# Optimization experiments

Measured on AMD Instinct MI355X. Metric: run time of the kernel, lower is better.

The kernel has to match this reference:

```python
import jax, jax.numpy as jnp
import numpy as np

B, T, D, H, L, V = 2, 1024, 1024, 4, 4, 32000  # H redefined below
H = 16            # n_heads
HD = D // H       # head_size = 64
NL = 4            # n_layer
EPS = 1e-5


def _layernorm(x, scale, bias):
    mu = jnp.mean(x, axis=-1, keepdims=True)
    var = jnp.mean(jnp.square(x - mu), axis=-1, keepdims=True)
    return (x - mu) * jax.lax.rsqrt(var + EPS) * scale + bias


def setup_inputs() -> dict:
    key = jax.random.key(0)
    ks = iter(jax.random.split(key, 40))
    s = lambda shape: jax.random.normal(next(ks), shape, jnp.float32) * 0.02
    inp = {
        'idx': jax.random.randint(next(ks), (B, T), 0, V),
        'tok_emb': s((V, D)),
        'pos_emb': s((T, D)),
        # per-layer stacked params (leading axis = layer)
        'Wq': s((NL, D, D)), 'Wk': s((NL, D, D)), 'Wv': s((NL, D, D)),
        'Wo': s((NL, D, D)), 'bo': jnp.zeros((NL, D), jnp.float32),
        'ln1_s': jnp.ones((NL, D), jnp.float32), 'ln1_b': jnp.zeros((NL, D), jnp.float32),
        'ln2_s': jnp.ones((NL, D), jnp.float32), 'ln2_b': jnp.zeros((NL, D), jnp.float32),
        'W1': s((NL, D, 4 * D)), 'b1': jnp.zeros((NL, 4 * D), jnp.float32),
        'W2': s((NL, 4 * D, D)), 'b2': jnp.zeros((NL, D), jnp.float32),
        'lnf_s': jnp.ones((D,), jnp.float32), 'lnf_b': jnp.zeros((D,), jnp.float32),
        'Wlm': s((D, V)), 'blm': jnp.zeros((V,), jnp.float32),
    }
    return inp


def reference(idx, tok_emb, pos_emb, Wq, Wk, Wv, Wo, bo,
              ln1_s, ln1_b, ln2_s, ln2_b, W1, b1, W2, b2,
              lnf_s, lnf_b, Wlm, blm):
    b, t = idx.shape
    x = tok_emb[idx] + pos_emb[None, :t]            # [B,T,D]
    causal = jnp.tril(jnp.ones((t, t), bool))        # [T,T]
    scale = 1.0 / np.sqrt(HD).astype(np.float32)
    for l in range(NL):
        h = _layernorm(x, ln1_s[l], ln1_b[l])
        q = (h @ Wq[l]).reshape(b, t, H, HD)
        k = (h @ Wk[l]).reshape(b, t, H, HD)
        v = (h @ Wv[l]).reshape(b, t, H, HD)
        scores = jnp.einsum('bthd,bshd->bhts', q, k) * scale
        scores = jnp.where(causal[None, None], scores, -jnp.inf)
        attn = jax.nn.softmax(scores, axis=-1)       # [B,H,T,T]
        o = jnp.einsum('bhts,bshd->bthd', attn, v).reshape(b, t, D)
        x = x + o @ Wo[l] + bo[l]
        h2 = _layernorm(x, ln2_s[l], ln2_b[l])
        x = x + jax.nn.relu(h2 @ W1[l] + b1[l]) @ W2[l] + b2[l]
    x = _layernorm(x, lnf_s, lnf_b)
    logits = x @ Wlm + blm                           # [B,T,V]
    return logits
```

## Files before the change

### kernel.cpp

```cpp
#include <hip/hip_runtime.h>

typedef unsigned short u16;
typedef unsigned int u32;
typedef __bf16 bf16x8 __attribute__((ext_vector_type(8)));
typedef float f32x4 __attribute__((ext_vector_type(4)));
typedef u16 u16x8 __attribute__((ext_vector_type(8)));
typedef u16 u16x4 __attribute__((ext_vector_type(4)));

static __device__ __forceinline__ u16 f2bf(float f) {
  u32 u = __builtin_bit_cast(u32, f);
  u32 r = (u + 0x7FFFu + ((u >> 16) & 1u)) >> 16;
  return (u16)r;
}

#define GLOAD_LDS16(gp, lp)                                                   \
  __builtin_amdgcn_global_load_lds(                                           \
      (const __attribute__((address_space(1))) void*)(gp),                    \
      (__attribute__((address_space(3))) void*)(lp), 16, 0, 0)

__global__ void k_embed(const int* __restrict__ idx, const float* __restrict__ tok,
                        const float* __restrict__ pos, float* __restrict__ x) {
  int row = blockIdx.x;
  int t = row & 1023;
  int id = idx[row];
  int c = threadIdx.x * 4;
  float4 a = *(const float4*)(tok + (size_t)id * 1024 + c);
  float4 p = *(const float4*)(pos + (size_t)t * 1024 + c);
  float4 r{a.x + p.x, a.y + p.y, a.z + p.z, a.w + p.w};
  *(float4*)(x + (size_t)row * 1024 + c) = r;
}

__global__ void k_ln(const float* __restrict__ x, const float* __restrict__ sc,
                     const float* __restrict__ bi, u16* __restrict__ out) {
  int row = blockIdx.x;
  int t = threadIdx.x;
  const float* xr = x + (size_t)row * 1024;
  float4 v = *(const float4*)(xr + t * 4);
  float s = v.x + v.y + v.z + v.w;
  float ss = v.x * v.x + v.y * v.y + v.z * v.z + v.w * v.w;
  for (int d = 1; d < 64; d <<= 1) { s += __shfl_xor(s, d); ss += __shfl_xor(ss, d); }
  __shared__ float red[8];
  int wave = t >> 6, lane = t & 63;
  if (lane == 0) { red[wave] = s; red[wave + 4] = ss; }
  __syncthreads();
  s = red[0] + red[1] + red[2] + red[3];
  ss = red[4] + red[5] + red[6] + red[7];
  float mu = s * (1.0f / 1024.0f);
  float var = ss * (1.0f / 1024.0f) - mu * mu;
  float inv = rsqrtf(var + 1e-5f);
  float4 g = *(const float4*)(sc + t * 4);
  float4 b = *(const float4*)(bi + t * 4);
  u16x4 o;
  o[0] = f2bf((v.x - mu) * inv * g.x + b.x);
  o[1] = f2bf((v.y - mu) * inv * g.y + b.y);
  o[2] = f2bf((v.z - mu) * inv * g.z + b.z);
  o[3] = f2bf((v.w - mu) * inv * g.w + b.w);
  *(u16x4*)(out + (size_t)row * 1024 + t * 4) = o;
}

__launch_bounds__(1024)
__global__ void k_transpose(const float* __restrict__ src, u16* __restrict__ dst,
                            int R, int C) {
  __shared__ float tile[32][33];
  int tx = threadIdx.x, ty = threadIdx.y;
  int c = blockIdx.x * 32 + tx;
  int r = blockIdx.y * 32 + ty;
  tile[ty][tx] = src[(size_t)r * C + c];
  __syncthreads();
  int dr = blockIdx.x * 32 + ty;
  int dc = blockIdx.y * 32 + tx;
  dst[(size_t)dr * R + dc] = f2bf(tile[tx][ty]);
}

__launch_bounds__(1024)
__global__ void k_transpose_layer(const float* __restrict__ Wq, const float* __restrict__ Wk,
                                  const float* __restrict__ Wv, const float* __restrict__ Wo,
                                  const float* __restrict__ W1, const float* __restrict__ W2,
                                  u16* __restrict__ qkvT, u16* __restrict__ WoT,
                                  u16* __restrict__ W1T, u16* __restrict__ W2T) {
  int bid = blockIdx.x;
  const float* src; u16* dst; int R, C, bx, by;
  if (bid < 4096) {
    int which = bid >> 10, tile_i = bid & 1023;
    bx = tile_i & 31; by = tile_i >> 5; R = 1024; C = 1024;
    src = which == 0 ? Wq : which == 1 ? Wk : which == 2 ? Wv : Wo;
    dst = which == 3 ? WoT : qkvT + (size_t)which * 1048576;
  } else if (bid < 8192) {
    int tile_i = bid - 4096; bx = tile_i & 127; by = tile_i >> 7; R = 1024; C = 4096;
    src = W1; dst = W1T;
  } else {
    int tile_i = bid - 8192; bx = tile_i & 31; by = tile_i >> 5; R = 4096; C = 1024;
    src = W2; dst = W2T;
  }
  __shared__ float tile[32][33];
  int tx = threadIdx.x, ty = threadIdx.y;
  int c = bx * 32 + tx, r = by * 32 + ty;
  tile[ty][tx] = src[(size_t)r * C + c];
  __syncthreads();
  int dr = bx * 32 + ty, dc = by * 32 + tx;
  dst[(size_t)dr * R + dc] = f2bf(tile[tx][ty]);
}

enum { EPI_QKV = 0, EPI_RES = 1, EPI_RELU = 2 };

template <int EPI>
__launch_bounds__(256, 4)
__global__ void k_gemm(const u16* __restrict__ A, const u16* __restrict__ Bt,
                       const float* __restrict__ bias, float* __restrict__ fout,
                       u16* __restrict__ bout, int M, int N, int K) {
  __shared__ alignas(16) u16 sm[2][2][128][32];
  const int t = threadIdx.x;
  const int wave = t >> 6, lane = t & 63;
  const int wm = wave >> 1, wn = wave & 1;
  const int g = lane >> 4, c = lane & 15;
  const int m0 = blockIdx.x * 128, n0 = blockIdx.y * 128;

  const int srow = wave * 32 + (lane >> 2);
  const int sseg = (lane & 3) * 8;
  const u16* gA = A + (size_t)(m0 + srow) * K + sseg;
  const u16* gB = Bt + (size_t)(n0 + srow) * K + sseg;

  f32x4 acc[4][4] = {};
  const int nK = K >> 5;
  int cur = 0;

#pragma unroll
  for (int p = 0; p < 2; ++p) {
    GLOAD_LDS16(gA + (size_t)p * 16 * K, &sm[0][0][wave * 32 + p * 16][0]);
    GLOAD_LDS16(gB + (size_t)p * 16 * K, &sm[0][1][wave * 32 + p * 16][0]);
  }
  __syncthreads();

  for (int kt = 0; kt < nK; ++kt) {
    if (kt + 1 < nK) {
      const int k0 = (kt + 1) << 5;
#pragma unroll
      for (int p = 0; p < 2; ++p) {
        GLOAD_LDS16(gA + k0 + (size_t)p * 16 * K, &sm[cur ^ 1][0][wave * 32 + p * 16][0]);
        GLOAD_LDS16(gB + k0 + (size_t)p * 16 * K, &sm[cur ^ 1][1][wave * 32 + p * 16][0]);
      }
    }
    bf16x8 af[4], bfr[4];
#pragma unroll
    for (int i = 0; i < 4; ++i) {
      af[i]  = *(const bf16x8*)&sm[cur][0][wm * 64 + i * 16 + c][g * 8];
      bfr[i] = *(const bf16x8*)&sm[cur][1][wn * 64 + i * 16 + c][g * 8];
    }
#pragma unroll
    for (int i = 0; i < 4; ++i)
#pragma unroll
      for (int j = 0; j < 4; ++j)
        acc[i][j] = __builtin_amdgcn_mfma_f32_16x16x32_bf16(af[i], bfr[j], acc[i][j], 0, 0, 0);
    __syncthreads();
    cur ^= 1;
  }

#pragma unroll
  for (int i = 0; i < 4; ++i)
#pragma unroll
    for (int j = 0; j < 4; ++j)
#pragma unroll
      for (int r = 0; r < 4; ++r) {
        int m = m0 + wm * 64 + i * 16 + g * 4 + r;
        int n = n0 + wn * 64 + j * 16 + c;
        float v = acc[i][j][r];
        if (EPI == EPI_RES) {
          fout[(size_t)m * N + n] += v + bias[n];
        } else if (EPI == EPI_RELU) {
          float u = v + bias[n];
          bout[(size_t)m * N + n] = f2bf(u > 0.f ? u : 0.f);
        }
      }
}

template <int EPI>
__launch_bounds__(256, 4)
__global__ void k_gemm64(const u16* __restrict__ A, const u16* __restrict__ Bt,
                         const float* __restrict__ bias, float* __restrict__ fout,
                         u16* __restrict__ bout, int M, int N, int K) {
  __shared__ alignas(16) u16 smem[12288];
#define AL(s, r, k) smem[(s)*2048 + (r)*32 + (k)]
#define BL(s, r, k) smem[4096 + (s)*4096 + (r)*32 + (k)]
  const int t = threadIdx.x;
  const int wave = t >> 6, lane = t & 63;
  const int wm = wave >> 1, wn = wave & 1;
  const int g = lane >> 4, c = lane & 15;
  const int m0 = blockIdx.x * 64, n0 = blockIdx.y * 128;

  const int rwA = t >> 2, sgA = (t & 3) * 8;
  const u16* gA = A + (size_t)(m0 + rwA) * K + sgA;
  const u16* gB = Bt + (size_t)(n0 + rwA) * K + sgA;

  f32x4 acc[2][4] = {};
  const int nK = K >> 5;
  int cur = 0;

  GLOAD_LDS16(gA, &AL(0, rwA, 0));
#pragma unroll
  for (int p = 0; p < 2; ++p)
    GLOAD_LDS16(gB + (size_t)p * 64 * K, &BL(0, p * 64 + rwA, 0));
  __syncthreads();

  for (int kt = 0; kt < nK; ++kt) {
    if (kt + 1 < nK) {
      const int k0 = (kt + 1) << 5;
      GLOAD_LDS16(gA + k0, &AL(cur ^ 1, rwA, 0));
#pragma unroll
      for (int p = 0; p < 2; ++p)
        GLOAD_LDS16(gB + k0 + (size_t)p * 64 * K, &BL(cur ^ 1, p * 64 + rwA, 0));
    }
    bf16x8 af[2], bfr[4];
#pragma unroll
    for (int i = 0; i < 2; ++i)
      af[i] = *(const bf16x8*)&AL(cur, wm * 32 + i * 16 + c, g * 8);
#pragma unroll
    for (int j = 0; j < 4; ++j)
      bfr[j] = *(const bf16x8*)&BL(cur, wn * 64 + j * 16 + c, g * 8);
#pragma unroll
    for (int i = 0; i < 2; ++i)
#pragma unroll
      for (int j = 0; j < 4; ++j)
        acc[i][j] = __builtin_amdgcn_mfma_f32_16x16x32_bf16(af[i], bfr[j], acc[i][j], 0, 0, 0);
    __syncthreads();
    cur ^= 1;
  }

  if (EPI == EPI_QKV) {
    u16 (*Ct)[136] = (u16(*)[136])smem;
#pragma unroll
    for (int i = 0; i < 2; ++i)
#pragma unroll
      for (int j = 0; j < 4; ++j)
#pragma unroll
        for (int r = 0; r < 4; ++r)
          Ct[wm * 32 + i * 16 + g * 4 + r][wn * 64 + j * 16 + c] = f2bf(acc[i][j][r]);
    __syncthreads();
    const int b = m0 >> 10, t0 = m0 & 1023;
    const int hh0 = (n0 >> 6) & 15, which = n0 >> 10;
    u16* obase = bout + (size_t)which * 2097152;
#pragma unroll
    for (int itr = 0; itr < 4; ++itr) {
      int idx2 = itr * 256 + t;
      int s = idx2 >> 9;
      int tt = (idx2 >> 3) & 63;
      int seg = idx2 & 7;
      u16x8 vv = *(const u16x8*)&Ct[tt][s * 64 + seg * 8];
      *(u16x8*)(obase + ((size_t)(b * 16 + hh0 + s) * 1024 + (t0 + tt)) * 64 + seg * 8) = vv;
    }
    return;
  }

#pragma unroll
  for (int i = 0; i < 2; ++i)
#pragma unroll
    for (int j = 0; j < 4; ++j)
#pragma unroll
      for (int r = 0; r < 4; ++r) {
        int m = m0 + wm * 32 + i * 16 + g * 4 + r;
        int n = n0 + wn * 64 + j * 16 + c;
        if (EPI == EPI_RES) fout[(size_t)m * N + n] += acc[i][j][r] + bias[n];
      }
#undef AL
#undef BL
}


#define BAR                                                                    \
  {                                                                            \
    asm volatile("" ::: "memory");                                             \
    __builtin_amdgcn_s_barrier();                                              \
    asm volatile("" ::: "memory");                                             \
  }
#define VM4 asm volatile("s_waitcnt vmcnt(4)" ::: "memory")
#define VM0 asm volatile("s_waitcnt vmcnt(0)" ::: "memory")

#define STGA(sl, hf, kt)                                                       \
  {                                                                            \
    _Pragma("unroll") for (int p = 0; p < 2; ++p) {                            \
      int idx = p * 512 + t, rw = idx >> 3, sg = idx & 7;                      \
      GLOAD_LDS16(A + (size_t)(m0 + (hf)*128 + rw) * K + (kt)*64 +             \
                      ((sg ^ (rw & 7)) << 3),                                  \
                  &Alds[sl][(hf)*128 + rw][sg << 3]);                          \
    }                                                                          \
  }
#define STGB(sl, hf, kt)                                                       \
  {                                                                            \
    _Pragma("unroll") for (int p = 0; p < 2; ++p) {                            \
      int idx = p * 512 + t, rw = idx >> 3, sg = idx & 7;                      \
      GLOAD_LDS16(Bt + (size_t)(n0 + (hf)*128 + rw) * K + (kt)*64 +            \
                      ((sg ^ (rw & 7)) << 3),                                  \
                  &Blds[sl][(hf)*128 + rw][sg << 3]);                          \
    }                                                                          \
  }

#define LMLOAD_A(sl, mh)                                                       \
  _Pragma("unroll") for (int i = 0; i < 4; ++i) {                              \
    int ra = (mh)*128 + wm * 64 + i * 16 + c;                                  \
    _Pragma("unroll") for (int ks = 0; ks < 2; ++ks)                           \
      af[i][ks] = *(const bf16x8*)&Alds[sl][ra][(((ks << 2) | g) ^ (ra & 7)) << 3]; \
  }
#define LMLOAD_B(sl, nh, bfv)                                                  \
  _Pragma("unroll") for (int j = 0; j < 2; ++j) {                              \
    int rb = (nh)*128 + wn * 32 + j * 16 + c;                                  \
    _Pragma("unroll") for (int ks = 0; ks < 2; ++ks)                           \
      bfv[j][ks] = *(const bf16x8*)&Blds[sl][rb][(((ks << 2) | g) ^ (rb & 7)) << 3]; \
  }
#define LMMMA(mh, nh, bfv)                                                     \
  __builtin_amdgcn_s_setprio(1);                                               \
  _Pragma("unroll") for (int i = 0; i < 4; ++i)                                \
    _Pragma("unroll") for (int j = 0; j < 2; ++j)                              \
      _Pragma("unroll") for (int ks = 0; ks < 2; ++ks)                         \
        acc[mh][nh][i][j] = __builtin_amdgcn_mfma_f32_16x16x32_bf16(           \
            af[i][ks], bfv[j][ks], acc[mh][nh][i][j], 0, 0, 0);                \
  __builtin_amdgcn_s_setprio(0);

__launch_bounds__(512, 2)
__global__ void k_gemm_lm(const u16* __restrict__ A, const u16* __restrict__ Bt,
                          const float* __restrict__ bias, float* __restrict__ fout,
                          int M, int N, int K) {
  __shared__ alignas(16) u16 Alds[2][256][64];
  __shared__ alignas(16) u16 Blds[2][256][64];
  const int t = threadIdx.x;
  const int wid = t >> 6, lane = t & 63;
  const int wm = wid >> 2, wn = wid & 3;
  const int g = lane >> 4, c = lane & 15;

  int bid = blockIdx.x;
  int swz = (bid & 7) * 125 + (bid >> 3);
  const int m0 = (swz & 7) * 256, n0 = (swz >> 3) * 256;

  f32x4 acc[2][2][4][2] = {};
  bf16x8 af[4][2], bf0[2][2], bf1[2][2];

  const int nK = K >> 6;
  const int nIter = nK >> 1;

  STGA(0, 0, 0); STGB(0, 0, 0);
  STGA(0, 1, 0); STGB(0, 1, 0);
  STGA(1, 0, 1); STGB(1, 0, 1);
  VM4;
  BAR;

  for (int it = 0; it < nIter; ++it) {
    const int t1 = 2 * it + 1, t2 = 2 * it + 2, t3 = 2 * it + 3;
    const bool more = (it + 1 < nIter);
    LMLOAD_A(0, 0); LMLOAD_B(0, 0, bf0);
    STGA(1, 1, t1); STGB(1, 1, t1);
    BAR; LMMMA(0, 0, bf0); BAR;
    LMLOAD_B(0, 1, bf1);
    BAR; LMMMA(0, 1, bf1); BAR;
    LMLOAD_A(0, 1);
    if (more) { STGA(0, 0, t2); }
    BAR; LMMMA(1, 1, bf1); BAR;
    if (more) { STGB(0, 0, t2); BAR; LMMMA(1, 0, bf0); VM4; BAR; }
    else      { BAR; LMMMA(1, 0, bf0); VM0; BAR; }
    LMLOAD_A(1, 0); LMLOAD_B(1, 0, bf0);
    if (more) { STGA(0, 1, t2); STGB(0, 1, t2); }
    BAR; LMMMA(0, 0, bf0); BAR;
    LMLOAD_B(1, 1, bf1);
    BAR; LMMMA(0, 1, bf1); BAR;
    LMLOAD_A(1, 1);
    if (more) { STGA(1, 0, t3); STGB(1, 0, t3); }
    BAR; LMMMA(1, 1, bf1); BAR;
    if (more) { BAR; LMMMA(1, 0, bf0); VM4; BAR; }
    else      { BAR; LMMMA(1, 0, bf0); VM0; BAR; }
  }

  float (*stile)[260] = (float(*)[260])&Alds[0][0][0];
#pragma unroll
  for (int RG = 0; RG < 8; ++RG) {
    const int mh = RG >> 2, wsel = (RG >> 1) & 1, ih = RG & 1;
    if (wm == wsel) {
#pragma unroll
      for (int i2 = 0; i2 < 2; ++i2)
#pragma unroll
        for (int nh = 0; nh < 2; ++nh)
#pragma unroll
          for (int j = 0; j < 2; ++j)
#pragma unroll
            for (int r = 0; r < 4; ++r) {
              float v = acc[mh][nh][ih * 2 + i2][j][r];
              stile[i2 * 16 + g * 4 + r][nh * 128 + wn * 32 + j * 16 + c] = v;
            }
    }
    __syncthreads();
    {
      int row = t >> 4, seg = t & 15;
      int m = m0 + RG * 32 + row;
      float* dst = fout + (size_t)m * N + n0 + seg * 16;
      const float* bsrc = bias + n0 + seg * 16;
#pragma unroll
      for (int q = 0; q < 4; ++q) {
        float4 v = *(const float4*)&stile[row][seg * 16 + q * 4];
        float4 bb = *(const float4*)&bsrc[q * 4];
        float4 o{v.x + bb.x, v.y + bb.y, v.z + bb.z, v.w + bb.w};
        *(float4*)(dst + q * 4) = o;
      }
    }
    __syncthreads();
  }
}

__launch_bounds__(64)
__global__ void k_attn(const u16* __restrict__ Q, const u16* __restrict__ Kb,
                       const u16* __restrict__ V, u16* __restrict__ O) {
  const int qb = blockIdx.x;
  const int bh = blockIdx.y;
  const int lane = threadIdx.x;
  const int g = lane >> 4, c = lane & 15;
  const int q0 = qb << 5;
  const u16* Qh = Q + (size_t)bh * 65536;
  const u16* Kh = Kb + (size_t)bh * 65536;
  const u16* Vh = V + (size_t)bh * 65536;

  __shared__ u16 Vt[64][40];
  __shared__ u16 Pl[32][40];

  bf16x8 aq[2][2];
#pragma unroll
  for (int qt = 0; qt < 2; ++qt) {
    aq[qt][0] = *(const bf16x8*)(Qh + (q0 + qt * 16 + c) * 64 + g * 8);
    aq[qt][1] = *(const bf16x8*)(Qh + (q0 + qt * 16 + c) * 64 + 32 + g * 8);
  }

  f32x4 Oacc[2][4] = {};
  float Mr[2][4], Lr[2][4] = {};
#pragma unroll
  for (int qt = 0; qt < 2; ++qt)
#pragma unroll
    for (int r = 0; r < 4; ++r) Mr[qt][r] = -1e30f;

  const int nIt = qb + 1;
  for (int it = 0; it < nIt; ++it) {
    const int k0 = it << 5;
    bf16x8 b0 = *(const bf16x8*)(Kh + (k0 + c) * 64 + g * 8);
    bf16x8 b1 = *(const bf16x8*)(Kh + (k0 + c) * 64 + 32 + g * 8);
    bf16x8 b2 = *(const bf16x8*)(Kh + (k0 + 16 + c) * 64 + g * 8);
    bf16x8 b3 = *(const bf16x8*)(Kh + (k0 + 16 + c) * 64 + 32 + g * 8);
    f32x4 S[2][2];
#pragma unroll
    for (int qt = 0; qt < 2; ++qt) {
      f32x4 z = {};
      S[qt][0] = __builtin_amdgcn_mfma_f32_16x16x32_bf16(
          aq[qt][1], b1, __builtin_amdgcn_mfma_f32_16x16x32_bf16(aq[qt][0], b0, z, 0, 0, 0), 0, 0, 0);
      S[qt][1] = __builtin_amdgcn_mfma_f32_16x16x32_bf16(
          aq[qt][1], b3, __builtin_amdgcn_mfma_f32_16x16x32_bf16(aq[qt][0], b2, z, 0, 0, 0), 0, 0, 0);
    }
#pragma unroll
    for (int p = 0; p < 4; ++p) {
      int key = (p << 3) + (lane >> 3);
      int d0 = (lane & 7) << 3;
      u16x8 vv = *(const u16x8*)(Vh + (size_t)(k0 + key) * 64 + d0);
#pragma unroll
      for (int j = 0; j < 8; ++j) Vt[d0 + j][key] = vv[j];
    }
    const float scale = 0.125f;
#pragma unroll
    for (int qt = 0; qt < 2; ++qt)
#pragma unroll
      for (int r = 0; r < 4; ++r) {
        int q = q0 + qt * 16 + (g << 2) + r;
        float s0 = (k0 + c <= q) ? S[qt][0][r] * scale : -1e30f;
        float s1 = (k0 + 16 + c <= q) ? S[qt][1][r] * scale : -1e30f;
        float m = fmaxf(s0, s1);
        m = fmaxf(m, __shfl_xor(m, 1));
        m = fmaxf(m, __shfl_xor(m, 2));
        m = fmaxf(m, __shfl_xor(m, 4));
        m = fmaxf(m, __shfl_xor(m, 8));
        float mnew = fmaxf(Mr[qt][r], m);
        float p0 = __expf(s0 - mnew);
        float p1 = __expf(s1 - mnew);
        float rs = p0 + p1;
        rs += __shfl_xor(rs, 1);
        rs += __shfl_xor(rs, 2);
        rs += __shfl_xor(rs, 4);
        rs += __shfl_xor(rs, 8);
        float alpha = __expf(Mr[qt][r] - mnew);
        Lr[qt][r] = Lr[qt][r] * alpha + rs;
        Mr[qt][r] = mnew;
#pragma unroll
        for (int nb = 0; nb < 4; ++nb) Oacc[qt][nb][r] *= alpha;
        Pl[qt * 16 + (g << 2) + r][c] = f2bf(p0);
        Pl[qt * 16 + (g << 2) + r][16 + c] = f2bf(p1);
      }
#pragma unroll
    for (int nb = 0; nb < 4; ++nb) {
      bf16x8 bv = *(const bf16x8*)&Vt[nb * 16 + c][g * 8];
#pragma unroll
      for (int qt = 0; qt < 2; ++qt) {
        bf16x8 ap = *(const bf16x8*)&Pl[qt * 16 + c][g * 8];
        Oacc[qt][nb] = __builtin_amdgcn_mfma_f32_16x16x32_bf16(ap, bv, Oacc[qt][nb], 0, 0, 0);
      }
    }
  }
  const int b = bh >> 4, hh = bh & 15;
#pragma unroll
  for (int qt = 0; qt < 2; ++qt)
#pragma unroll
    for (int r = 0; r < 4; ++r) {
      int tt = q0 + qt * 16 + (g << 2) + r;
      float invl = 1.0f / Lr[qt][r];
#pragma unroll
      for (int nb = 0; nb < 4; ++nb) {
        int d = nb * 16 + c;
        O[((size_t)(b * 1024 + tt)) * 1024 + hh * 64 + d] = f2bf(Oacc[qt][nb][r] * invl);
      }
    }
}

extern "C" void kernel_launch(void* const* d_in, const int* in_sizes, int n_in,
                              void* d_out, int out_size, void* d_ws, size_t ws_size,
                              hipStream_t stream) {
  const int*   idx  = (const int*)d_in[0];
  const float* tok  = (const float*)d_in[1];
  const float* pos  = (const float*)d_in[2];
  const float* Wq   = (const float*)d_in[3];
  const float* Wk   = (const float*)d_in[4];
  const float* Wv   = (const float*)d_in[5];
  const float* Wo   = (const float*)d_in[6];
  const float* bo   = (const float*)d_in[7];
  const float* ln1s = (const float*)d_in[8];
  const float* ln1b = (const float*)d_in[9];
  const float* ln2s = (const float*)d_in[10];
  const float* ln2b = (const float*)d_in[11];
  const float* W1   = (const float*)d_in[12];
  const float* b1   = (const float*)d_in[13];
  const float* W2   = (const float*)d_in[14];
  const float* b2   = (const float*)d_in[15];
  const float* lnfs = (const float*)d_in[16];
  const float* lnfb = (const float*)d_in[17];
  const float* Wlm  = (const float*)d_in[18];
  const float* blm  = (const float*)d_in[19];
  float* out = (float*)d_out;

  char* w = (char*)d_ws;
  auto alloc = [&](size_t bytes) {
    char* p = w;
    w += (bytes + 255) & ~(size_t)255;
    return p;
  };
  float* x  = (float*)alloc(2048ull * 1024 * 4);
  u16* h    = (u16*)alloc(2048ull * 1024 * 2);
  u16* qkv  = (u16*)alloc(3ull * 2097152 * 2);
  u16* o    = (u16*)alloc(2048ull * 1024 * 2);
  u16* a1   = (u16*)alloc(2048ull * 4096 * 2);
  u16* arena = (u16*)alloc(32000ull * 1024 * 2);

  dim3 b32(32, 32, 1);

  k_embed<<<2048, 256, 0, stream>>>(idx, tok, pos, x);

  for (int l = 0; l < 4; ++l) {
    u16* qkvT = arena;
    u16* WoT  = arena + 3ull * 1048576;
    u16* W1T  = arena + 4ull * 1048576;
    u16* W2T  = arena + 8ull * 1048576;
    k_transpose_layer<<<12288, b32, 0, stream>>>(
        Wq + (size_t)l * 1048576, Wk + (size_t)l * 1048576,
        Wv + (size_t)l * 1048576, Wo + (size_t)l * 1048576,
        W1 + (size_t)l * 4194304, W2 + (size_t)l * 4194304,
        qkvT, WoT, W1T, W2T);

    k_ln<<<2048, 256, 0, stream>>>(x, ln1s + l * 1024, ln1b + l * 1024, h);
    k_gemm64<EPI_QKV><<<dim3(32, 24), 256, 0, stream>>>(h, qkvT, nullptr, nullptr, qkv,
                                                        2048, 3072, 1024);
    k_attn<<<dim3(32, 32), 64, 0, stream>>>(qkv, qkv + 2097152, qkv + 2 * 2097152, o);
    k_gemm64<EPI_RES><<<dim3(32, 8), 256, 0, stream>>>(o, WoT, bo + l * 1024, x, nullptr,
                                                       2048, 1024, 1024);
    k_ln<<<2048, 256, 0, stream>>>(x, ln2s + l * 1024, ln2b + l * 1024, h);
    k_gemm<EPI_RELU><<<dim3(16, 32), 256, 0, stream>>>(h, W1T, b1 + l * 4096, nullptr, a1,
                                                       2048, 4096, 1024);
    k_gemm64<EPI_RES><<<dim3(32, 8), 256, 0, stream>>>(a1, W2T, b2 + l * 1024, x, nullptr,
                                                       2048, 1024, 4096);
  }

  k_ln<<<2048, 256, 0, stream>>>(x, lnfs, lnfb, h);
  k_transpose<<<dim3(1000, 32), b32, 0, stream>>>(Wlm, arena, 1024, 32000);
  k_gemm_lm<<<1000, 512, 0, stream>>>(h, arena, blm, out, 2048, 32000, 1024);
}
```

Measured before the change: 1.270 ms.

## Retile GEMMs, replace LM-head kernel, add lazy softmax rescale in attention

The hand-pipelined 256x256 LM-head GEMM with 512 threads is replaced by a simpler 128x128 double-buffered kernel that writes logits through an LDS-staged epilogue. The residual GEMMs (Wo and W2) move to a new 64x64-tile kernel so twice as many blocks cover the small N=1024 output. The W1 ReLU GEMM moves to the 64x128 kernel with an LDS-staged, vectorised bf16 store. Attention skips the running-max update and the output rescale when no row's max has grown by more than 8, trading some exponent headroom for fewer exp and multiply operations. Several independent changes carry different risks; the simpler LM-head kernel is the largest and may be slower than the tuned version it replaces.

```diff
diff --git a/kernel.cpp b/kernel.cpp
--- a/kernel.cpp
+++ b/kernel.cpp
@@ -101,83 +101,13 @@
   dst[(size_t)dr * R + dc] = f2bf(tile[tx][ty]);
 }
 
-enum { EPI_QKV = 0, EPI_RES = 1, EPI_RELU = 2 };
-
-template <int EPI>
-__launch_bounds__(256, 4)
-__global__ void k_gemm(const u16* __restrict__ A, const u16* __restrict__ Bt,
-                       const float* __restrict__ bias, float* __restrict__ fout,
-                       u16* __restrict__ bout, int M, int N, int K) {
-  __shared__ alignas(16) u16 sm[2][2][128][32];
-  const int t = threadIdx.x;
-  const int wave = t >> 6, lane = t & 63;
-  const int wm = wave >> 1, wn = wave & 1;
-  const int g = lane >> 4, c = lane & 15;
-  const int m0 = blockIdx.x * 128, n0 = blockIdx.y * 128;
-
-  const int srow = wave * 32 + (lane >> 2);
-  const int sseg = (lane & 3) * 8;
-  const u16* gA = A + (size_t)(m0 + srow) * K + sseg;
-  const u16* gB = Bt + (size_t)(n0 + srow) * K + sseg;
-
-  f32x4 acc[4][4] = {};
-  const int nK = K >> 5;
-  int cur = 0;
-
-#pragma unroll
-  for (int p = 0; p < 2; ++p) {
-    GLOAD_LDS16(gA + (size_t)p * 16 * K, &sm[0][0][wave * 32 + p * 16][0]);
-    GLOAD_LDS16(gB + (size_t)p * 16 * K, &sm[0][1][wave * 32 + p * 16][0]);
-  }
-  __syncthreads();
-
-  for (int kt = 0; kt < nK; ++kt) {
-    if (kt + 1 < nK) {
-      const int k0 = (kt + 1) << 5;
-#pragma unroll
-      for (int p = 0; p < 2; ++p) {
-        GLOAD_LDS16(gA + k0 + (size_t)p * 16 * K, &sm[cur ^ 1][0][wave * 32 + p * 16][0]);
-        GLOAD_LDS16(gB + k0 + (size_t)p * 16 * K, &sm[cur ^ 1][1][wave * 32 + p * 16][0]);
-      }
-    }
-    bf16x8 af[4], bfr[4];
-#pragma unroll
-    for (int i = 0; i < 4; ++i) {
-      af[i]  = *(const bf16x8*)&sm[cur][0][wm * 64 + i * 16 + c][g * 8];
-      bfr[i] = *(const bf16x8*)&sm[cur][1][wn * 64 + i * 16 + c][g * 8];
-    }
-#pragma unroll
-    for (int i = 0; i < 4; ++i)
-#pragma unroll
-      for (int j = 0; j < 4; ++j)
-        acc[i][j] = __builtin_amdgcn_mfma_f32_16x16x32_bf16(af[i], bfr[j], acc[i][j], 0, 0, 0);
-    __syncthreads();
-    cur ^= 1;
-  }
-
-#pragma unroll
-  for (int i = 0; i < 4; ++i)
-#pragma unroll
-    for (int j = 0; j < 4; ++j)
-#pragma unroll
-      for (int r = 0; r < 4; ++r) {
-        int m = m0 + wm * 64 + i * 16 + g * 4 + r;
-        int n = n0 + wn * 64 + j * 16 + c;
-        float v = acc[i][j][r];
-        if (EPI == EPI_RES) {
-          fout[(size_t)m * N + n] += v + bias[n];
-        } else if (EPI == EPI_RELU) {
-          float u = v + bias[n];
-          bout[(size_t)m * N + n] = f2bf(u > 0.f ? u : 0.f);
-        }
-      }
-}
+enum { EPI_QKV = 0, EPI_RELU = 2 };
 
 template <int EPI>
 __launch_bounds__(256, 4)
 __global__ void k_gemm64(const u16* __restrict__ A, const u16* __restrict__ Bt,
-                         const float* __restrict__ bias, float* __restrict__ fout,
-                         u16* __restrict__ bout, int M, int N, int K) {
+                         const float* __restrict__ bias, u16* __restrict__ bout,
+                         int M, int N, int K) {
   __shared__ alignas(16) u16 smem[12288];
 #define AL(s, r, k) smem[(s)*2048 + (r)*32 + (k)]
 #define BL(s, r, k) smem[4096 + (s)*4096 + (r)*32 + (k)]
@@ -247,152 +177,156 @@
       u16x8 vv = *(const u16x8*)&Ct[tt][s * 64 + seg * 8];
       *(u16x8*)(obase + ((size_t)(b * 16 + hh0 + s) * 1024 + (t0 + tt)) * 64 + seg * 8) = vv;
     }
-    return;
+  } else {
+    u16 (*Ct)[136] = (u16(*)[136])smem;
+#pragma unroll
+    for (int i = 0; i < 2; ++i)
+#pragma unroll
+      for (int j = 0; j < 4; ++j)
+#pragma unroll
+        for (int r = 0; r < 4; ++r) {
+          float u = acc[i][j][r] + bias[n0 + wn * 64 + j * 16 + c];
+          Ct[wm * 32 + i * 16 + g * 4 + r][wn * 64 + j * 16 + c] = f2bf(u > 0.f ? u : 0.f);
+        }
+    __syncthreads();
+#pragma unroll
+    for (int itr = 0; itr < 4; ++itr) {
+      int idx2 = itr * 256 + t;
+      int tt = idx2 >> 4, seg = idx2 & 15;
+      *(u16x8*)(bout + (size_t)(m0 + tt) * N + n0 + seg * 8) =
+          *(const u16x8*)&Ct[tt][seg * 8];
+    }
+  }
+#undef AL
+#undef BL
+}
+
+__launch_bounds__(256, 8)
+__global__ void k_gemm_res(const u16* __restrict__ A, const u16* __restrict__ Bt,
+                           const float* __restrict__ bias, float* __restrict__ fout,
+                           int M, int N, int K) {
+  __shared__ alignas(16) u16 smem[8192];
+  const int t = threadIdx.x;
+  const int wave = t >> 6, lane = t & 63;
+  const int wm = wave >> 1, wn = wave & 1;
+  const int g = lane >> 4, c = lane & 15;
+  const int m0 = blockIdx.x * 64, n0 = blockIdx.y * 64;
+
+  const int rw = t >> 2, sg = (t & 3) * 8;
+  const u16* gA = A + (size_t)(m0 + rw) * K + sg;
+  const u16* gB = Bt + (size_t)(n0 + rw) * K + sg;
+
+  f32x4 acc[2][2] = {};
+  const int nK = K >> 5;
+  int cur = 0;
+
+  GLOAD_LDS16(gA, &smem[rw * 32]);
+  GLOAD_LDS16(gB, &smem[4096 + rw * 32]);
+  __syncthreads();
+
+  for (int kt = 0; kt < nK; ++kt) {
+    if (kt + 1 < nK) {
+      const int k0 = (kt + 1) << 5;
+      GLOAD_LDS16(gA + k0, &smem[(cur ^ 1) * 2048 + rw * 32]);
+      GLOAD_LDS16(gB + k0, &smem[4096 + (cur ^ 1) * 2048 + rw * 32]);
+    }
+    bf16x8 af[2], bfr[2];
+#pragma unroll
+    for (int i = 0; i < 2; ++i)
+      af[i] = *(const bf16x8*)&smem[cur * 2048 + (wm * 32 + i * 16 + c) * 32 + g * 8];
+#pragma unroll
+    for (int j = 0; j < 2; ++j)
+      bfr[j] = *(const bf16x8*)&smem[4096 + cur * 2048 + (wn * 32 + j * 16 + c) * 32 + g * 8];
+#pragma unroll
+    for (int i = 0; i < 2; ++i)
+#pragma unroll
+      for (int j = 0; j < 2; ++j)
+        acc[i][j] = __builtin_amdgcn_mfma_f32_16x16x32_bf16(af[i], bfr[j], acc[i][j], 0, 0, 0);
+    __syncthreads();
+    cur ^= 1;
   }
 
 #pragma unroll
   for (int i = 0; i < 2; ++i)
 #pragma unroll
-    for (int j = 0; j < 4; ++j)
+    for (int j = 0; j < 2; ++j)
 #pragma unroll
       for (int r = 0; r < 4; ++r) {
         int m = m0 + wm * 32 + i * 16 + g * 4 + r;
-        int n = n0 + wn * 64 + j * 16 + c;
-        if (EPI == EPI_RES) fout[(size_t)m * N + n] += acc[i][j][r] + bias[n];
-      }
-#undef AL
-#undef BL
-}
-
-
-#define BAR                                                                    \
-  {                                                                            \
-    asm volatile("" ::: "memory");                                             \
-    __builtin_amdgcn_s_barrier();                                              \
-    asm volatile("" ::: "memory");                                             \
-  }
-#define VM4 asm volatile("s_waitcnt vmcnt(4)" ::: "memory")
-#define VM0 asm volatile("s_waitcnt vmcnt(0)" ::: "memory")
-
-#define STGA(sl, hf, kt)                                                       \
-  {                                                                            \
-    _Pragma("unroll") for (int p = 0; p < 2; ++p) {                            \
-      int idx = p * 512 + t, rw = idx >> 3, sg = idx & 7;                      \
-      GLOAD_LDS16(A + (size_t)(m0 + (hf)*128 + rw) * K + (kt)*64 +             \
-                      ((sg ^ (rw & 7)) << 3),                                  \
-                  &Alds[sl][(hf)*128 + rw][sg << 3]);                          \
-    }                                                                          \
-  }
-#define STGB(sl, hf, kt)                                                       \
-  {                                                                            \
-    _Pragma("unroll") for (int p = 0; p < 2; ++p) {                            \
-      int idx = p * 512 + t, rw = idx >> 3, sg = idx & 7;                      \
-      GLOAD_LDS16(Bt + (size_t)(n0 + (hf)*128 + rw) * K + (kt)*64 +            \
-                      ((sg ^ (rw & 7)) << 3),                                  \
-                  &Blds[sl][(hf)*128 + rw][sg << 3]);                          \
-    }                                                                          \
-  }
-
-#define LMLOAD_A(sl, mh)                                                       \
-  _Pragma("unroll") for (int i = 0; i < 4; ++i) {                              \
-    int ra = (mh)*128 + wm * 64 + i * 16 + c;                                  \
-    _Pragma("unroll") for (int ks = 0; ks < 2; ++ks)                           \
-      af[i][ks] = *(const bf16x8*)&Alds[sl][ra][(((ks << 2) | g) ^ (ra & 7)) << 3]; \
-  }
-#define LMLOAD_B(sl, nh, bfv)                                                  \
-  _Pragma("unroll") for (int j = 0; j < 2; ++j) {                              \
-    int rb = (nh)*128 + wn * 32 + j * 16 + c;                                  \
-    _Pragma("unroll") for (int ks = 0; ks < 2; ++ks)                           \
-      bfv[j][ks] = *(const bf16x8*)&Blds[sl][rb][(((ks << 2) | g) ^ (rb & 7)) << 3]; \
-  }
-#define LMMMA(mh, nh, bfv)                                                     \
-  __builtin_amdgcn_s_setprio(1);                                               \
-  _Pragma("unroll") for (int i = 0; i < 4; ++i)                                \
-    _Pragma("unroll") for (int j = 0; j < 2; ++j)                              \
-      _Pragma("unroll") for (int ks = 0; ks < 2; ++ks)                         \
-        acc[mh][nh][i][j] = __builtin_amdgcn_mfma_f32_16x16x32_bf16(           \
-            af[i][ks], bfv[j][ks], acc[mh][nh][i][j], 0, 0, 0);                \
-  __builtin_amdgcn_s_setprio(0);
-
-__launch_bounds__(512, 2)
-__global__ void k_gemm_lm(const u16* __restrict__ A, const u16* __restrict__ Bt,
-                          const float* __restrict__ bias, float* __restrict__ fout,
-                          int M, int N, int K) {
-  __shared__ alignas(16) u16 Alds[2][256][64];
-  __shared__ alignas(16) u16 Blds[2][256][64];
+        int n = n0 + wn * 32 + j * 16 + c;
+        fout[(size_t)m * N + n] += acc[i][j][r] + bias[n];
+      }
+}
+
+__launch_bounds__(256, 5)
+__global__ void k_gemm_out(const u16* __restrict__ A, const u16* __restrict__ Bt,
+                           const float* __restrict__ bias, float* __restrict__ fout,
+                           int M, int N, int K) {
+  __shared__ alignas(16) u16 sm[2][2][128][32];
   const int t = threadIdx.x;
-  const int wid = t >> 6, lane = t & 63;
-  const int wm = wid >> 2, wn = wid & 3;
+  const int wave = t >> 6, lane = t & 63;
+  const int wm = wave >> 1, wn = wave & 1;
   const int g = lane >> 4, c = lane & 15;
-
-  int bid = blockIdx.x;
-  int swz = (bid & 7) * 125 + (bid >> 3);
-  const int m0 = (swz & 7) * 256, n0 = (swz >> 3) * 256;
-
-  f32x4 acc[2][2][4][2] = {};
-  bf16x8 af[4][2], bf0[2][2], bf1[2][2];
-
-  const int nK = K >> 6;
-  const int nIter = nK >> 1;
-
-  STGA(0, 0, 0); STGB(0, 0, 0);
-  STGA(0, 1, 0); STGB(0, 1, 0);
-  STGA(1, 0, 1); STGB(1, 0, 1);
-  VM4;
-  BAR;
-
-  for (int it = 0; it < nIter; ++it) {
-    const int t1 = 2 * it + 1, t2 = 2 * it + 2, t3 = 2 * it + 3;
-    const bool more = (it + 1 < nIter);
-    LMLOAD_A(0, 0); LMLOAD_B(0, 0, bf0);
-    STGA(1, 1, t1); STGB(1, 1, t1);
-    BAR; LMMMA(0, 0, bf0); BAR;
-    LMLOAD_B(0, 1, bf1);
-    BAR; LMMMA(0, 1, bf1); BAR;
-    LMLOAD_A(0, 1);
-    if (more) { STGA(0, 0, t2); }
-    BAR; LMMMA(1, 1, bf1); BAR;
-    if (more) { STGB(0, 0, t2); BAR; LMMMA(1, 0, bf0); VM4; BAR; }
-    else      { BAR; LMMMA(1, 0, bf0); VM0; BAR; }
-    LMLOAD_A(1, 0); LMLOAD_B(1, 0, bf0);
-    if (more) { STGA(0, 1, t2); STGB(0, 1, t2); }
-    BAR; LMMMA(0, 0, bf0); BAR;
-    LMLOAD_B(1, 1, bf1);
-    BAR; LMMMA(0, 1, bf1); BAR;
-    LMLOAD_A(1, 1);
-    if (more) { STGA(1, 0, t3); STGB(1, 0, t3); }
-    BAR; LMMMA(1, 1, bf1); BAR;
-    if (more) { BAR; LMMMA(1, 0, bf0); VM4; BAR; }
-    else      { BAR; LMMMA(1, 0, bf0); VM0; BAR; }
-  }
-
-  float (*stile)[260] = (float(*)[260])&Alds[0][0][0];
-#pragma unroll
-  for (int RG = 0; RG < 8; ++RG) {
-    const int mh = RG >> 2, wsel = (RG >> 1) & 1, ih = RG & 1;
-    if (wm == wsel) {
-#pragma unroll
-      for (int i2 = 0; i2 < 2; ++i2)
-#pragma unroll
-        for (int nh = 0; nh < 2; ++nh)
-#pragma unroll
-          for (int j = 0; j < 2; ++j)
-#pragma unroll
-            for (int r = 0; r < 4; ++r) {
-              float v = acc[mh][nh][ih * 2 + i2][j][r];
-              stile[i2 * 16 + g * 4 + r][nh * 128 + wn * 32 + j * 16 + c] = v;
-            }
-    }
+  const int m0 = blockIdx.x * 128, n0 = blockIdx.y * 128;
+
+  const int srow = wave * 32 + (lane >> 2);
+  const int sseg = (lane & 3) * 8;
+  const u16* gA = A + (size_t)(m0 + srow) * K + sseg;
+  const u16* gB = Bt + (size_t)(n0 + srow) * K + sseg;
+
+  f32x4 acc[4][4] = {};
+  const int nK = K >> 5;
+  int cur = 0;
+
+#pragma unroll
+  for (int p = 0; p < 2; ++p) {
+    GLOAD_LDS16(gA + (size_t)p * 16 * K, &sm[0][0][wave * 32 + p * 16][0]);
+    GLOAD_LDS16(gB + (size_t)p * 16 * K, &sm[0][1][wave * 32 + p * 16][0]);
+  }
+  __syncthreads();
+
+  for (int kt = 0; kt < nK; ++kt) {
+    if (kt + 1 < nK) {
+      const int k0 = (kt + 1) << 5;
+#pragma unroll
+      for (int p = 0; p < 2; ++p) {
+        GLOAD_LDS16(gA + k0 + (size_t)p * 16 * K, &sm[cur ^ 1][0][wave * 32 + p * 16][0]);
+        GLOAD_LDS16(gB + k0 + (size_t)p * 16 * K, &sm[cur ^ 1][1][wave * 32 + p * 16][0]);
+      }
+    }
+    bf16x8 af[4], bfr[4];
+#pragma unroll
+    for (int i = 0; i < 4; ++i) {
+      af[i]  = *(const bf16x8*)&sm[cur][0][wm * 64 + i * 16 + c][g * 8];
+      bfr[i] = *(const bf16x8*)&sm[cur][1][wn * 64 + i * 16 + c][g * 8];
+    }
+#pragma unroll
+    for (int i = 0; i < 4; ++i)
+#pragma unroll
+      for (int j = 0; j < 4; ++j)
+        acc[i][j] = __builtin_amdgcn_mfma_f32_16x16x32_bf16(af[i], bfr[j], acc[i][j], 0, 0, 0);
+    __syncthreads();
+    cur ^= 1;
+  }
+
+  float (*st)[132] = (float(*)[132])sm;
+#pragma unroll
+  for (int i = 0; i < 4; ++i) {
+#pragma unroll
+    for (int j = 0; j < 4; ++j)
+#pragma unroll
+      for (int r = 0; r < 4; ++r)
+        st[wm * 16 + g * 4 + r][wn * 64 + j * 16 + c] = acc[i][j][r];
     __syncthreads();
     {
-      int row = t >> 4, seg = t & 15;
-      int m = m0 + RG * 32 + row;
-      float* dst = fout + (size_t)m * N + n0 + seg * 16;
-      const float* bsrc = bias + n0 + seg * 16;
+      int row = t >> 3;
+      int cs = (t & 7) * 16;
+      int m = m0 + (row >> 4) * 64 + i * 16 + (row & 15);
+      float* dst = fout + (size_t)m * N + n0 + cs;
 #pragma unroll
       for (int q = 0; q < 4; ++q) {
-        float4 v = *(const float4*)&stile[row][seg * 16 + q * 4];
-        float4 bb = *(const float4*)&bsrc[q * 4];
+        float4 v = *(const float4*)&st[row][cs + q * 4];
+        float4 bb = *(const float4*)&bias[n0 + cs + q * 4];
         float4 o{v.x + bb.x, v.y + bb.y, v.z + bb.z, v.w + bb.w};
         *(float4*)(dst + q * 4) = o;
       }
@@ -455,6 +389,8 @@
       for (int j = 0; j < 8; ++j) Vt[d0 + j][key] = vv[j];
     }
     const float scale = 0.125f;
+    float sv[2][2][4], mt[2][4];
+    float need = 0.0f;
 #pragma unroll
     for (int qt = 0; qt < 2; ++qt)
 #pragma unroll
@@ -462,24 +398,37 @@
         int q = q0 + qt * 16 + (g << 2) + r;
         float s0 = (k0 + c <= q) ? S[qt][0][r] * scale : -1e30f;
         float s1 = (k0 + 16 + c <= q) ? S[qt][1][r] * scale : -1e30f;
+        sv[qt][0][r] = s0; sv[qt][1][r] = s1;
         float m = fmaxf(s0, s1);
         m = fmaxf(m, __shfl_xor(m, 1));
         m = fmaxf(m, __shfl_xor(m, 2));
         m = fmaxf(m, __shfl_xor(m, 4));
         m = fmaxf(m, __shfl_xor(m, 8));
-        float mnew = fmaxf(Mr[qt][r], m);
-        float p0 = __expf(s0 - mnew);
-        float p1 = __expf(s1 - mnew);
+        mt[qt][r] = m;
+        need = fmaxf(need, m - Mr[qt][r]);
+      }
+    const bool nore = __all(need <= 8.0f);
+#pragma unroll
+    for (int qt = 0; qt < 2; ++qt)
+#pragma unroll
+      for (int r = 0; r < 4; ++r) {
+        float mn = nore ? Mr[qt][r] : fmaxf(Mr[qt][r], mt[qt][r]);
+        float p0 = __expf(sv[qt][0][r] - mn);
+        float p1 = __expf(sv[qt][1][r] - mn);
         float rs = p0 + p1;
         rs += __shfl_xor(rs, 1);
         rs += __shfl_xor(rs, 2);
         rs += __shfl_xor(rs, 4);
         rs += __shfl_xor(rs, 8);
-        float alpha = __expf(Mr[qt][r] - mnew);
-        Lr[qt][r] = Lr[qt][r] * alpha + rs;
-        Mr[qt][r] = mnew;
-#pragma unroll
-        for (int nb = 0; nb < 4; ++nb) Oacc[qt][nb][r] *= alpha;
+        if (nore) {
+          Lr[qt][r] += rs;
+        } else {
+          float alpha = __expf(Mr[qt][r] - mn);
+          Lr[qt][r] = Lr[qt][r] * alpha + rs;
+          Mr[qt][r] = mn;
+#pragma unroll
+          for (int nb = 0; nb < 4; ++nb) Oacc[qt][nb][r] *= alpha;
+        }
         Pl[qt * 16 + (g << 2) + r][c] = f2bf(p0);
         Pl[qt * 16 + (g << 2) + r][16 + c] = f2bf(p1);
       }
@@ -562,19 +511,19 @@
         qkvT, WoT, W1T, W2T);
 
     k_ln<<<2048, 256, 0, stream>>>(x, ln1s + l * 1024, ln1b + l * 1024, h);
-    k_gemm64<EPI_QKV><<<dim3(32, 24), 256, 0, stream>>>(h, qkvT, nullptr, nullptr, qkv,
+    k_gemm64<EPI_QKV><<<dim3(32, 24), 256, 0, stream>>>(h, qkvT, nullptr, qkv,
                                                         2048, 3072, 1024);
     k_attn<<<dim3(32, 32), 64, 0, stream>>>(qkv, qkv + 2097152, qkv + 2 * 2097152, o);
-    k_gemm64<EPI_RES><<<dim3(32, 8), 256, 0, stream>>>(o, WoT, bo + l * 1024, x, nullptr,
-                                                       2048, 1024, 1024);
+    k_gemm_res<<<dim3(32, 16), 256, 0, stream>>>(o, WoT, bo + l * 1024, x,
+                                                 2048, 1024, 1024);
     k_ln<<<2048, 256, 0, stream>>>(x, ln2s + l * 1024, ln2b + l * 1024, h);
-    k_gemm<EPI_RELU><<<dim3(16, 32), 256, 0, stream>>>(h, W1T, b1 + l * 4096, nullptr, a1,
-                                                       2048, 4096, 1024);
-    k_gemm64<EPI_RES><<<dim3(32, 8), 256, 0, stream>>>(a1, W2T, b2 + l * 1024, x, nullptr,
-                                                       2048, 1024, 4096);
+    k_gemm64<EPI_RELU><<<dim3(32, 32), 256, 0, stream>>>(h, W1T, b1 + l * 4096, a1,
+                                                         2048, 4096, 1024);
+    k_gemm_res<<<dim3(32, 16), 256, 0, stream>>>(a1, W2T, b2 + l * 1024, x,
+                                                 2048, 1024, 4096);
   }
 
   k_ln<<<2048, 256, 0, stream>>>(x, lnfs, lnfb, h);
   k_transpose<<<dim3(1000, 32), b32, 0, stream>>>(Wlm, arena, 1024, 32000);
-  k_gemm_lm<<<1000, 512, 0, stream>>>(h, arena, blm, out, 2048, 32000, 1024);
-}
+  k_gemm_out<<<dim3(16, 250), 256, 0, stream>>>(h, arena, blm, out, 2048, 32000, 1024);
+}
```

Result: slower. 1.348 ms (+6.1%).
